# Kernel tuning notes

Measured on AMD Instinct MI355X. Metric: run time of the kernel, lower is better.

The kernel has to match this reference:

```python
import jax, jax.numpy as jnp
import numpy as np

TEMPERATURE = 2.0 / 3.0
LIMIT_A = -0.1
LIMIT_B = 1.1

N_NODES = 50000
N_CLUSTERS = 64
N_RELATIONS = 8
N_EDGES = 1000000


def setup_inputs() -> dict:
    key = jax.random.key(0)
    ks = jax.random.split(key, 6)
    xavier = float(np.sqrt(6.0 / (N_CLUSTERS + N_CLUSTERS)))
    return {
        "assignments": jax.random.normal(ks[0], (N_NODES, N_CLUSTERS), jnp.float32),
        "inter_cluster_logits": jax.random.uniform(ks[1], (N_RELATIONS, N_CLUSTERS, N_CLUSTERS), jnp.float32, -xavier, xavier),
        "log_alpha": jnp.zeros((N_RELATIONS, N_CLUSTERS, N_CLUSTERS), jnp.float32),
        "absent_bias": jnp.zeros((N_RELATIONS,), jnp.float32),
        "edge_index": jax.random.randint(ks[2], (2, N_EDGES), 0, N_NODES, jnp.int32),
        "edge_type": jax.random.randint(ks[3], (N_EDGES,), 0, N_RELATIONS, jnp.int32),
        "neg_edge_index": jax.random.randint(ks[4], (2, N_EDGES), 0, N_NODES, jnp.int32),
        "neg_edge_type": jax.random.randint(ks[5], (N_EDGES,), 0, N_RELATIONS, jnp.int32),
    }


def _edge_logits(assignments, weights, absent_bias, edge_index, edge_type):
    # src, dst: [E, C] gathers (irregular access)
    src = assignments[edge_index[0]]
    dst = assignments[edge_index[1]]
    n_rel = weights.shape[0]
    # torch.bmm(W[et], dst[:, :, None]) == dst @ W[et].T ; compute per relation
    # (fixed small relation loop; avoids materializing [E, C, C]) then select.
    logits_all = jnp.stack(
        [jnp.sum(src * (dst @ weights[r].T), axis=-1) for r in range(n_rel)],
        axis=-1,
    )  # [E, R]
    logits = jnp.take_along_axis(logits_all, edge_type[:, None], axis=1)[:, 0]
    return logits + absent_bias[edge_type]


def reference(assignments, inter_cluster_logits, log_alpha, absent_bias,
              edge_index, edge_type, neg_edge_index, neg_edge_type):
    # Hard-concrete gate, eval mode: z = clamp(sigmoid(log_alpha)*(b-a)+a, 0, 1)
    gate = jnp.clip(jax.nn.sigmoid(log_alpha) * (LIMIT_B - LIMIT_A) + LIMIT_A, 0.0, 1.0)
    weights = jax.nn.sigmoid(inter_cluster_logits) * gate  # [R, C, C]

    pos_logits = _edge_logits(assignments, weights, absent_bias, edge_index, edge_type)
    neg_logits = _edge_logits(assignments, weights, absent_bias, neg_edge_index, neg_edge_type)

    # BCE-with-logits: target=1 -> softplus(-x); target=0 -> softplus(x)
    pos_loss = jnp.mean(jax.nn.softplus(-pos_logits))
    neg_loss = jnp.mean(jax.nn.softplus(neg_logits))
    return pos_loss + neg_loss
```

## Files before the change

### kernel.cpp

```cpp
#include <hip/hip_runtime.h>
#include <hip/hip_bf16.h>
#include <math.h>

#define E_EDGES 1000000
#define N_NODES 50000
#define N_C     64
#define N_REL   8
#define CHB     2048
#define CAP     384
#define NBLK    489
#define BT      512

typedef __attribute__((ext_vector_type(4))) float floatx4;
typedef __attribute__((ext_vector_type(2))) float floatx2;

static __device__ __forceinline__ unsigned pk4_fp8(float a, float b, float c, float d) {
    unsigned w = 0;
    w = __builtin_amdgcn_cvt_pk_fp8_f32(a, b, w, false);
    w = __builtin_amdgcn_cvt_pk_fp8_f32(c, d, w, true);
    return w;
}

static __device__ __forceinline__ long long pack64(unsigned lo, unsigned hi) {
    uint2 u; u.x = lo; u.y = hi;
    return __builtin_bit_cast(long long, u);
}

__global__ __launch_bounds__(256) void prep_kernel(
    const float* __restrict__ assign,
    const float* __restrict__ icl,
    const float* __restrict__ la,
    unsigned char* __restrict__ Wp8,
    unsigned char* __restrict__ AS8,
    float* __restrict__ out)
{
    int tid = blockIdx.x * blockDim.x + threadIdx.x;
    int nth = gridDim.x * blockDim.x;
    if (tid == 0) out[0] = 0.0f;

    for (int idx = tid; idx < N_REL * N_C * 16; idx += nth) {
        int row = idx >> 4, dq = idx & 15;
        int q = dq >> 2, c = (dq >> 1) & 1, jh = dq & 1;
        int k0 = (2 * c + jh) * 16 + 4 * q;
        float wv[4];
        #pragma unroll
        for (int b = 0; b < 4; ++b) {
            int srci = (row << 6) + k0 + b;
            float w = 1.0f / (1.0f + __expf(-icl[srci]));
            float g = 1.0f / (1.0f + __expf(-la[srci])) * 1.2f - 0.1f;
            g = fminf(fmaxf(g, 0.0f), 1.0f);
            wv[b] = w * g;
        }
        ((unsigned*)Wp8)[idx] = pk4_fp8(wv[0], wv[1], wv[2], wv[3]);
    }

    for (int n = tid; n < N_NODES; n += nth) {
        const float4* a4 = (const float4*)(assign + (size_t)n * N_C);
        unsigned w[16];
        #pragma unroll
        for (int i = 0; i < 16; ++i) {
            float4 v = a4[i];
            w[i] = pk4_fp8(v.x, v.y, v.z, v.w);
        }
        uint4* as = (uint4*)(AS8 + (size_t)n * N_C);
        #pragma unroll
        for (int q = 0; q < 4; ++q) {
            uint4 o;
            o.x = w[0 * 4 + q];
            o.y = w[1 * 4 + q];
            o.z = w[2 * 4 + q];
            o.w = w[3 * 4 + q];
            as[q] = o;
        }
    }
}

__global__ __launch_bounds__(BT, 8) void edge_kernel(
    const unsigned char* __restrict__ AS8,
    const unsigned char* __restrict__ Wp8,
    const float* __restrict__ absent_bias,
    const int* __restrict__ ei, const int* __restrict__ et,
    const int* __restrict__ nei, const int* __restrict__ net,
    float* __restrict__ out)
{
    __shared__ unsigned list[N_REL * CAP];
    __shared__ unsigned cnt[N_REL];
    __shared__ float red[8];
    if (threadIdx.x < N_REL) cnt[threadIdx.x] = 0u;
    __syncthreads();

    int blk = blockIdx.x;
    bool isneg = blk >= NBLK;
    int lb = isneg ? blk - NBLK : blk;
    const int* Es = isneg ? nei : ei;
    const int* Et = isneg ? net : et;
    float sign = isneg ? 1.0f : -1.0f;
    int base = lb * CHB;
    int elim = min(base + CHB, E_EDGES);

    for (int e = base + threadIdx.x; e < elim; e += BT) {
        int s = Es[e];
        int d = Es[E_EDGES + e];
        int r = Et[e];
        unsigned rank = atomicAdd(&cnt[r], 1u);
        if (rank < CAP) list[r * CAP + rank] = (unsigned)s | ((unsigned)d << 16);
    }
    __syncthreads();

    int lane = threadIdx.x & 63;
    int wid  = threadIdx.x >> 6;
    int n16  = lane & 15;
    int quad = lane >> 4;
    float loss = 0.0f;

    for (int r = 0; r < N_REL; ++r) {
        int n_r = min((int)cnt[r], CAP);
        if (n_r == 0) continue;
        float bias = absent_bias[r];
        uint4 wfm[4];
        #pragma unroll
        for (int mt = 0; mt < 4; ++mt)
            wfm[mt] = *(const uint4*)(Wp8 + ((r * 64 + mt * 16 + n16) << 6) + quad * 16);

        int g = wid;
        bool valid = false;
        uint4 S = {0, 0, 0, 0}, D = {0, 0, 0, 0};
        if (g * 16 < n_r) {
            int idx = g * 16 + n16;
            valid = idx < n_r;
            unsigned rec = list[r * CAP + (valid ? idx : 0)];
            S = *(const uint4*)(AS8 + ((size_t)(rec & 0xFFFF) << 6) + quad * 16);
            D = *(const uint4*)(AS8 + ((size_t)(rec >> 16) << 6) + quad * 16);
        }
        while (g * 16 < n_r) {
            int g2 = g + 8;
            bool valid2 = false;
            uint4 S2 = {0, 0, 0, 0}, D2 = {0, 0, 0, 0};
            if (g2 * 16 < n_r) {
                int idx2 = g2 * 16 + n16;
                valid2 = idx2 < n_r;
                unsigned rec2 = list[r * CAP + (valid2 ? idx2 : 0)];
                S2 = *(const uint4*)(AS8 + ((size_t)(rec2 & 0xFFFF) << 6) + quad * 16);
                D2 = *(const uint4*)(AS8 + ((size_t)(rec2 >> 16) << 6) + quad * 16);
            }

            long long bD0 = pack64(D.x, D.y);
            long long bD1 = pack64(D.z, D.w);
            floatx4 ac[4];
            #pragma unroll
            for (int mt = 0; mt < 4; ++mt) {
                floatx4 z = {0.0f, 0.0f, 0.0f, 0.0f};
                z = __builtin_amdgcn_mfma_f32_16x16x32_fp8_fp8(
                        pack64(wfm[mt].x, wfm[mt].y), bD0, z, 0, 0, 0);
                ac[mt] = __builtin_amdgcn_mfma_f32_16x16x32_fp8_fp8(
                        pack64(wfm[mt].z, wfm[mt].w), bD1, z, 0, 0, 0);
            }
            unsigned sw[4] = {S.x, S.y, S.z, S.w};
            float d0 = 0.0f, d1 = 0.0f;
            #pragma unroll
            for (int mt = 0; mt < 4; mt += 2) {
                floatx2 lo0 = __builtin_amdgcn_cvt_pk_f32_fp8((int)sw[mt], false);
                floatx2 hi0 = __builtin_amdgcn_cvt_pk_f32_fp8((int)sw[mt], true);
                floatx2 lo1 = __builtin_amdgcn_cvt_pk_f32_fp8((int)sw[mt + 1], false);
                floatx2 hi1 = __builtin_amdgcn_cvt_pk_f32_fp8((int)sw[mt + 1], true);
                d0 = fmaf(lo0.x, ac[mt][0], d0);
                d1 = fmaf(lo1.x, ac[mt + 1][0], d1);
                d0 = fmaf(lo0.y, ac[mt][1], d0);
                d1 = fmaf(lo1.y, ac[mt + 1][1], d1);
                d0 = fmaf(hi0.x, ac[mt][2], d0);
                d1 = fmaf(hi1.x, ac[mt + 1][2], d1);
                d0 = fmaf(hi0.y, ac[mt][3], d0);
                d1 = fmaf(hi1.y, ac[mt + 1][3], d1);
            }
            float dot = d0 + d1;
            dot += __shfl_xor(dot, 16);
            dot += __shfl_xor(dot, 32);
            if (quad == 0 && valid) {
                float x = sign * (dot + bias);
                loss += fmaxf(x, 0.0f) + __logf(1.0f + __expf(-fabsf(x)));
            }

            g = g2; valid = valid2; S = S2; D = D2;
        }
    }

    loss += __shfl_xor(loss, 1);
    loss += __shfl_xor(loss, 2);
    loss += __shfl_xor(loss, 4);
    loss += __shfl_xor(loss, 8);
    loss += __shfl_xor(loss, 16);
    loss += __shfl_xor(loss, 32);
    if (lane == 0) red[wid] = loss;
    __syncthreads();
    if (threadIdx.x == 0) {
        float t = red[0] + red[1] + red[2] + red[3]
                + red[4] + red[5] + red[6] + red[7];
        atomicAdd(out, t * (1.0f / (float)E_EDGES));
    }
}

extern "C" void kernel_launch(void* const* d_in, const int* in_sizes, int n_in,
                              void* d_out, int out_size, void* d_ws, size_t ws_size,
                              hipStream_t stream) {
    const float* assign = (const float*)d_in[0];
    const float* icl    = (const float*)d_in[1];
    const float* la     = (const float*)d_in[2];
    const float* ab     = (const float*)d_in[3];
    const int*   ei     = (const int*)d_in[4];
    const int*   et     = (const int*)d_in[5];
    const int*   nei    = (const int*)d_in[6];
    const int*   net    = (const int*)d_in[7];
    float* out = (float*)d_out;

    char* basep = (char*)d_ws;
    unsigned char* Wp8 = (unsigned char*)basep;
    unsigned char* AS8 = (unsigned char*)(basep + 65536);

    prep_kernel<<<256, 256, 0, stream>>>(assign, icl, la, Wp8, AS8, out);
    edge_kernel<<<2 * NBLK, BT, 0, stream>>>(AS8, Wp8, ab, ei, et, nei, net, out);
}
```

Before: 134.9 us.

## Flatten relation groups into one balanced work range per wave with sentinel padding

```diff
diff --git a/kernel.cpp b/kernel.cpp
--- a/kernel.cpp
+++ b/kernel.cpp
@@ -10,6 +10,7 @@
 #define CAP     384
 #define NBLK    489
 #define BT      512
+#define SENT    0xFFFFFFFFu
 
 typedef __attribute__((ext_vector_type(4))) float floatx4;
 typedef __attribute__((ext_vector_type(2))) float floatx2;
@@ -107,81 +108,132 @@
     }
     __syncthreads();
 
+    if (threadIdx.x < N_REL * 16) {
+        int r = threadIdx.x >> 4;
+        int i = threadIdx.x & 15;
+        int n = min((int)cnt[r], CAP);
+        int padded = ((n + 15) >> 4) << 4;
+        int slot = n + i;
+        if (slot < padded) list[r * CAP + slot] = SENT;
+    }
+    __syncthreads();
+
     int lane = threadIdx.x & 63;
     int wid  = threadIdx.x >> 6;
     int n16  = lane & 15;
     int quad = lane >> 4;
     float loss = 0.0f;
 
-    for (int r = 0; r < N_REL; ++r) {
-        int n_r = min((int)cnt[r], CAP);
-        if (n_r == 0) continue;
-        float bias = absent_bias[r];
-        uint4 wfm[4];
+    int G0 = (min((int)cnt[0], CAP) + 15) >> 4;
+    int G1 = (min((int)cnt[1], CAP) + 15) >> 4;
+    int G2 = (min((int)cnt[2], CAP) + 15) >> 4;
+    int G3 = (min((int)cnt[3], CAP) + 15) >> 4;
+    int G4 = (min((int)cnt[4], CAP) + 15) >> 4;
+    int G5 = (min((int)cnt[5], CAP) + 15) >> 4;
+    int G6 = (min((int)cnt[6], CAP) + 15) >> 4;
+    int G7 = (min((int)cnt[7], CAP) + 15) >> 4;
+    int go1 = G0;
+    int go2 = go1 + G1;
+    int go3 = go2 + G2;
+    int go4 = go3 + G3;
+    int go5 = go4 + G4;
+    int go6 = go5 + G5;
+    int go7 = go6 + G6;
+    int tg  = go7 + G7;
+
+    #define LOCATE(ITEM, R, GOF)                                   \
+        do {                                                       \
+            R = 0; GOF = 0;                                        \
+            if ((ITEM) >= go1) { R = 1; GOF = go1; }               \
+            if ((ITEM) >= go2) { R = 2; GOF = go2; }               \
+            if ((ITEM) >= go3) { R = 3; GOF = go3; }               \
+            if ((ITEM) >= go4) { R = 4; GOF = go4; }               \
+            if ((ITEM) >= go5) { R = 5; GOF = go5; }               \
+            if ((ITEM) >= go6) { R = 6; GOF = go6; }               \
+            if ((ITEM) >= go7) { R = 7; GOF = go7; }               \
+        } while (0)
+
+    #define FETCH(ITEM, R, V, SREG, DREG)                                    \
+        do {                                                                 \
+            int gof_;                                                        \
+            LOCATE(ITEM, R, gof_);                                           \
+            unsigned rec_ = list[R * CAP + ((ITEM) - gof_) * 16 + n16];      \
+            V = rec_ != SENT;                                                \
+            unsigned sm_ = V ? (rec_ & 0xFFFFu) : 0u;                        \
+            unsigned dm_ = V ? (rec_ >> 16) : 0u;                            \
+            SREG = *(const uint4*)(AS8 + ((size_t)sm_ << 6) + quad * 16);    \
+            DREG = *(const uint4*)(AS8 + ((size_t)dm_ << 6) + quad * 16);    \
+        } while (0)
+
+    int start = (wid * tg) >> 3;
+    int end   = ((wid + 1) * tg) >> 3;
+
+    int rC = 0;
+    bool vC = false;
+    uint4 SC = {0, 0, 0, 0}, DC = {0, 0, 0, 0};
+    uint4 wfm[4];
+    float bias = 0.0f;
+
+    if (start < end) {
+        FETCH(start, rC, vC, SC, DC);
         #pragma unroll
         for (int mt = 0; mt < 4; ++mt)
-            wfm[mt] = *(const uint4*)(Wp8 + ((r * 64 + mt * 16 + n16) << 6) + quad * 16);
-
-        int g = wid;
-        bool valid = false;
-        uint4 S = {0, 0, 0, 0}, D = {0, 0, 0, 0};
-        if (g * 16 < n_r) {
-            int idx = g * 16 + n16;
-            valid = idx < n_r;
-            unsigned rec = list[r * CAP + (valid ? idx : 0)];
-            S = *(const uint4*)(AS8 + ((size_t)(rec & 0xFFFF) << 6) + quad * 16);
-            D = *(const uint4*)(AS8 + ((size_t)(rec >> 16) << 6) + quad * 16);
-        }
-        while (g * 16 < n_r) {
-            int g2 = g + 8;
-            bool valid2 = false;
-            uint4 S2 = {0, 0, 0, 0}, D2 = {0, 0, 0, 0};
-            if (g2 * 16 < n_r) {
-                int idx2 = g2 * 16 + n16;
-                valid2 = idx2 < n_r;
-                unsigned rec2 = list[r * CAP + (valid2 ? idx2 : 0)];
-                S2 = *(const uint4*)(AS8 + ((size_t)(rec2 & 0xFFFF) << 6) + quad * 16);
-                D2 = *(const uint4*)(AS8 + ((size_t)(rec2 >> 16) << 6) + quad * 16);
-            }
-
-            long long bD0 = pack64(D.x, D.y);
-            long long bD1 = pack64(D.z, D.w);
-            floatx4 ac[4];
+            wfm[mt] = *(const uint4*)(Wp8 + ((rC * 64 + mt * 16 + n16) << 6) + quad * 16);
+        bias = absent_bias[rC];
+    }
+
+    for (int it = start; it < end; ++it) {
+        int rN = rC;
+        bool vN = false;
+        uint4 SN = {0, 0, 0, 0}, DN = {0, 0, 0, 0};
+        if (it + 1 < end) {
+            FETCH(it + 1, rN, vN, SN, DN);
+        }
+
+        long long bD0 = pack64(DC.x, DC.y);
+        long long bD1 = pack64(DC.z, DC.w);
+        floatx4 ac[4];
+        #pragma unroll
+        for (int mt = 0; mt < 4; ++mt) {
+            floatx4 z = {0.0f, 0.0f, 0.0f, 0.0f};
+            z = __builtin_amdgcn_mfma_f32_16x16x32_fp8_fp8(
+                    pack64(wfm[mt].x, wfm[mt].y), bD0, z, 0, 0, 0);
+            ac[mt] = __builtin_amdgcn_mfma_f32_16x16x32_fp8_fp8(
+                    pack64(wfm[mt].z, wfm[mt].w), bD1, z, 0, 0, 0);
+        }
+        unsigned sw[4] = {SC.x, SC.y, SC.z, SC.w};
+        float d0 = 0.0f, d1 = 0.0f;
+        #pragma unroll
+        for (int mt = 0; mt < 4; mt += 2) {
+            floatx2 lo0 = __builtin_amdgcn_cvt_pk_f32_fp8((int)sw[mt], false);
+            floatx2 hi0 = __builtin_amdgcn_cvt_pk_f32_fp8((int)sw[mt], true);
+            floatx2 lo1 = __builtin_amdgcn_cvt_pk_f32_fp8((int)sw[mt + 1], false);
+            floatx2 hi1 = __builtin_amdgcn_cvt_pk_f32_fp8((int)sw[mt + 1], true);
+            d0 = fmaf(lo0.x, ac[mt][0], d0);
+            d1 = fmaf(lo1.x, ac[mt + 1][0], d1);
+            d0 = fmaf(lo0.y, ac[mt][1], d0);
+            d1 = fmaf(lo1.y, ac[mt + 1][1], d1);
+            d0 = fmaf(hi0.x, ac[mt][2], d0);
+            d1 = fmaf(hi1.x, ac[mt + 1][2], d1);
+            d0 = fmaf(hi0.y, ac[mt][3], d0);
+            d1 = fmaf(hi1.y, ac[mt + 1][3], d1);
+        }
+        float dot = d0 + d1;
+        dot += __shfl_xor(dot, 16);
+        dot += __shfl_xor(dot, 32);
+        if (quad == 0 && vC) {
+            float x = sign * (dot + bias);
+            loss += fmaxf(x, 0.0f) + __logf(1.0f + __expf(-fabsf(x)));
+        }
+
+        if (rN != rC) {
             #pragma unroll
-            for (int mt = 0; mt < 4; ++mt) {
-                floatx4 z = {0.0f, 0.0f, 0.0f, 0.0f};
-                z = __builtin_amdgcn_mfma_f32_16x16x32_fp8_fp8(
-                        pack64(wfm[mt].x, wfm[mt].y), bD0, z, 0, 0, 0);
-                ac[mt] = __builtin_amdgcn_mfma_f32_16x16x32_fp8_fp8(
-                        pack64(wfm[mt].z, wfm[mt].w), bD1, z, 0, 0, 0);
-            }
-            unsigned sw[4] = {S.x, S.y, S.z, S.w};
-            float d0 = 0.0f, d1 = 0.0f;
-            #pragma unroll
-            for (int mt = 0; mt < 4; mt += 2) {
-                floatx2 lo0 = __builtin_amdgcn_cvt_pk_f32_fp8((int)sw[mt], false);
-                floatx2 hi0 = __builtin_amdgcn_cvt_pk_f32_fp8((int)sw[mt], true);
-                floatx2 lo1 = __builtin_amdgcn_cvt_pk_f32_fp8((int)sw[mt + 1], false);
-                floatx2 hi1 = __builtin_amdgcn_cvt_pk_f32_fp8((int)sw[mt + 1], true);
-                d0 = fmaf(lo0.x, ac[mt][0], d0);
-                d1 = fmaf(lo1.x, ac[mt + 1][0], d1);
-                d0 = fmaf(lo0.y, ac[mt][1], d0);
-                d1 = fmaf(lo1.y, ac[mt + 1][1], d1);
-                d0 = fmaf(hi0.x, ac[mt][2], d0);
-                d1 = fmaf(hi1.x, ac[mt + 1][2], d1);
-                d0 = fmaf(hi0.y, ac[mt][3], d0);
-                d1 = fmaf(hi1.y, ac[mt + 1][3], d1);
-            }
-            float dot = d0 + d1;
-            dot += __shfl_xor(dot, 16);
-            dot += __shfl_xor(dot, 32);
-            if (quad == 0 && valid) {
-                float x = sign * (dot + bias);
-                loss += fmaxf(x, 0.0f) + __logf(1.0f + __expf(-fabsf(x)));
-            }
-
-            g = g2; valid = valid2; S = S2; D = D2;
-        }
+            for (int mt = 0; mt < 4; ++mt)
+                wfm[mt] = *(const uint4*)(Wp8 + ((rN * 64 + mt * 16 + n16) << 6) + quad * 16);
+            bias = absent_bias[rN];
+            rC = rN;
+        }
+        vC = vN; SC = SN; DC = DN;
     }
 
     loss += __shfl_xor(loss, 1);
```

Measured after the change: 133.7 us. Within noise of the previous version (-0.8%).
